# Kernel optimization log

Hardware: AMD Instinct MI355X
Metric: run time of the kernel (lower is better)

The kernel has to match this reference:

```python
import jax, jax.numpy as jnp
import numpy as np

BATCH, T, N = 64, 512, 1024

def setup_inputs() -> dict:
    key = jax.random.key(0)
    k1, k2, k3 = jax.random.split(key, 3)
    input_sequence = jax.random.normal(k1, (BATCH, T, N), dtype=jnp.float32)
    W_self_lower = jax.random.normal(k2, (N, N), dtype=jnp.float32) * 0.1
    W_input = jax.random.normal(k3, (N, N), dtype=jnp.float32) * 0.1
    return {"input_sequence": input_sequence, "W_self_lower": W_self_lower, "W_input": W_input}

def reference(input_sequence, W_self_lower, W_input):
    # W_self symmetric: (W + W.T)/2; note W_self.T == W_self
    W_self = (W_self_lower + W_self_lower.T) * 0.5
    batch = input_sequence.shape[0]
    n = W_self.shape[0]
    # Precompute input projection for all timesteps: (B, T, N) @ (N, N)^T
    x_proj = jnp.einsum('btn,mn->btm', input_sequence, W_input)
    h0 = jnp.zeros((batch, n), dtype=input_sequence.dtype)

    def step(h, xp_t):
        h_new = jnp.tanh(h @ W_self.T + xp_t)
        return h_new, h_new

    # scan over time axis: move T to leading axis
    _, states = jax.lax.scan(step, h0, jnp.swapaxes(x_proj, 0, 1))
    return jnp.swapaxes(states, 0, 1)  # (B, T, N)
```

## Files before the change

kernel.cpp:

```cpp
#include <hip/hip_runtime.h>
#include <hip/hip_bf16.h>
#include <cstdint>
#include <cmath>

constexpr int BATCH = 64;
constexpr int T     = 512;
constexpr int N     = 1024;
constexpr int NWG   = 256;
constexpr int NG    = 32;
constexpr int GM    = 16;

typedef float f4 __attribute__((ext_vector_type(4)));
typedef short bs8 __attribute__((ext_vector_type(8)));

struct alignas(128) PadInt { int v; int pad[31]; };
__device__ PadInt g_cnt[NG];
__device__ PadInt g_flag[NG];

__device__ __forceinline__ f4 ld_sys_x4(const float* p) {
  f4 v;
  asm volatile("global_load_dwordx4 %0, %1, off sc0 sc1" : "=v"(v) : "v"(p));
  return v;
}
__device__ __forceinline__ int ld_sys_i32(const int* p) {
  int v;
  asm volatile("global_load_dword %0, %1, off sc0 sc1\n\ts_waitcnt vmcnt(0)"
               : "=v"(v) : "v"(p) : "memory");
  return v;
}
__device__ __forceinline__ void st_sys_f32(float* p, float v) {
  asm volatile("global_store_dword %0, %1, off sc0 sc1 nt" ::"v"(p), "v"(v)
               : "memory");
}
__device__ __forceinline__ void wait_vm0(void) {
  asm volatile("s_waitcnt vmcnt(0)" ::: "memory");
  __builtin_amdgcn_sched_barrier(0);
}

__device__ __forceinline__ void arrive_cnt(int g, int t) {
  int old = __hip_atomic_fetch_add(&g_cnt[g].v, 1, __ATOMIC_RELAXED,
                                   __HIP_MEMORY_SCOPE_AGENT);
  if (old == t * GM + (GM - 1))
    __hip_atomic_store(&g_flag[g].v, t + 1, __ATOMIC_RELAXED,
                       __HIP_MEMORY_SCOPE_AGENT);
}
__device__ __forceinline__ void pollf(int g, int e) {
  while (ld_sys_i32(&g_flag[g].v) < e) __builtin_amdgcn_s_sleep(1);
}

__device__ __forceinline__ unsigned short f2bf(float f) {
  unsigned u = __builtin_bit_cast(unsigned, f);
  u = u + 0x7FFFu + ((u >> 16) & 1u);
  return (unsigned short)(u >> 16);
}
__device__ __forceinline__ float bf2f(unsigned short b) {
  unsigned u = ((unsigned)b) << 16;
  return __builtin_bit_cast(float, u);
}
__device__ __forceinline__ bs8 mk8hi(const float* p) {
  bs8 r;
#pragma unroll
  for (int j = 0; j < 8; ++j) r[j] = (short)f2bf(p[j]);
  return r;
}
__device__ __forceinline__ void mk8hilo(const float* p, bs8& hi, bs8& lo) {
  f4 a = *reinterpret_cast<const f4*>(p);
  f4 b = *reinterpret_cast<const f4*>(p + 4);
  float v[8] = {a[0], a[1], a[2], a[3], b[0], b[1], b[2], b[3]};
#pragma unroll
  for (int j = 0; j < 8; ++j) {
    unsigned short h = f2bf(v[j]);
    hi[j] = (short)h;
    lo[j] = (short)f2bf(v[j] - bf2f(h));
  }
}

__global__ __launch_bounds__(256) void symm_k(const float* __restrict__ W,
                                              float* __restrict__ Ws) {
  if (blockIdx.x == 0 && blockIdx.y == 0 && threadIdx.x < NG) {
    __hip_atomic_store(&g_cnt[threadIdx.x].v, 0, __ATOMIC_RELAXED,
                       __HIP_MEMORY_SCOPE_AGENT);
    __hip_atomic_store(&g_flag[threadIdx.x].v, 0, __ATOMIC_RELAXED,
                       __HIP_MEMORY_SCOPE_AGENT);
  }
  int j = blockIdx.x * 16 + (threadIdx.x & 15);
  int i = blockIdx.y * 16 + (threadIdx.x >> 4);
  Ws[(size_t)i * N + j] = 0.5f * (W[(size_t)i * N + j] + W[(size_t)j * N + i]);
}

__global__ __launch_bounds__(256) void xproj_gemm(const float* __restrict__ A,
                                                  const float* __restrict__ B,
                                                  float* __restrict__ C,
                                                  int M) {
  constexpr int BM = 128, BN = 128, BK = 16;
  __shared__ float As[BK][BM + 4];
  __shared__ float Bs[BK][BN + 4];

  const int tid = threadIdx.x;
  const int lin = blockIdx.x + gridDim.x * blockIdx.y;
  const int sw  = ((lin & 7) << 8) + (lin >> 3);
  const int bm  = sw >> 3;
  const int bn  = sw & 7;
  const int tx = tid & 15, ty = tid >> 4;
  const int K = N;

  float acc[8][8];
#pragma unroll
  for (int i = 0; i < 8; ++i)
#pragma unroll
    for (int j = 0; j < 8; ++j) acc[i][j] = 0.f;

  for (int kt = 0; kt < K; kt += BK) {
#pragma unroll
    for (int s = 0; s < 2; ++s) {
      int f = tid + s * 256;
      int row = f >> 2, kq = f & 3;
      float4 a = *reinterpret_cast<const float4*>(
          &A[(size_t)(bm * BM + row) * K + kt + kq * 4]);
      As[kq * 4 + 0][row] = a.x;
      As[kq * 4 + 1][row] = a.y;
      As[kq * 4 + 2][row] = a.z;
      As[kq * 4 + 3][row] = a.w;
      float4 b = *reinterpret_cast<const float4*>(
          &B[(size_t)(bn * BN + row) * K + kt + kq * 4]);
      Bs[kq * 4 + 0][row] = b.x;
      Bs[kq * 4 + 1][row] = b.y;
      Bs[kq * 4 + 2][row] = b.z;
      Bs[kq * 4 + 3][row] = b.w;
    }
    __syncthreads();

#pragma unroll
    for (int k = 0; k < BK; ++k) {
      float a[8], b[8];
      *reinterpret_cast<float4*>(&a[0]) =
          *reinterpret_cast<const float4*>(&As[k][ty * 8]);
      *reinterpret_cast<float4*>(&a[4]) =
          *reinterpret_cast<const float4*>(&As[k][ty * 8 + 4]);
      *reinterpret_cast<float4*>(&b[0]) =
          *reinterpret_cast<const float4*>(&Bs[k][tx * 8]);
      *reinterpret_cast<float4*>(&b[4]) =
          *reinterpret_cast<const float4*>(&Bs[k][tx * 8 + 4]);
#pragma unroll
      for (int i = 0; i < 8; ++i)
#pragma unroll
        for (int j = 0; j < 8; ++j) acc[i][j] = fmaf(a[i], b[j], acc[i][j]);
    }
    __syncthreads();
  }

#pragma unroll
  for (int i = 0; i < 8; ++i) {
    size_t row = (size_t)bm * BM + ty * 8 + i;
#pragma unroll
    for (int j = 0; j < 8; j += 4) {
      *reinterpret_cast<float4*>(&C[row * N + bn * BN + tx * 8 + j]) =
          *reinterpret_cast<const float4*>(&acc[i][j]);
    }
  }
}

__global__ __launch_bounds__(640, 1) void rnn_persist(
    float* __restrict__ out, const float* __restrict__ Ws) {
  const int tid = threadIdx.x;
  const int wg  = blockIdx.x;
  const int p   = wg & 15;
  const int cg  = wg >> 4;
  const int m0  = cg * 64;
  const int gA  = 2 * p, gB = 2 * p + 1;
  const int b0A = gA * 2, b0B = gB * 2;
  const size_t TN = (size_t)T * N;

  __shared__ __align__(16) short wloL[64][1032];
  __shared__ __align__(16) float hA[2][1028];
  __shared__ __align__(16) float hB[2][1028];
  __shared__ float xplA[128], xplB[128];
  __shared__ float redA[8 * 128], redB[8 * 128];
  __shared__ int lflags[64];

  if (tid == 0) {
    lflags[0] = -1; lflags[16] = -1;
    lflags[8] = 0;  lflags[24] = 0;
    lflags[32] = 0; lflags[48] = 0;
  }

  const int l = tid & 63;
  const int v = tid >> 6;

  for (int e = tid; e < 64 * 1024; e += 640) {
    int row = e >> 10, k = e & 1023;
    float x = Ws[(size_t)(m0 + row) * N + k];
    unsigned short hi = f2bf(x);
    wloL[row][k] = (short)f2bf(x - bf2f(hi));
  }
  bs8 whi[4][4];
  if (v < 8) {
#pragma unroll
    for (int mt = 0; mt < 4; ++mt)
#pragma unroll
      for (int kt = 0; kt < 4; ++kt)
        whi[mt][kt] = mk8hi(
            &Ws[(size_t)(m0 + 16 * mt + (l & 15)) * N + 128 * v + 32 * kt +
                8 * (l >> 4)]);
  }
  __syncthreads();

  if (v < 8) {
    const int n = l & 15;
    const int koff = 128 * v + 8 * (l >> 4);

    auto do_chain = [&](float (*hX)[1028], float* xplX, float* redX,
                        int rdyIdx, int wsIdx, int ackIdx, int b0, int t) {
      while (*(volatile int*)&lflags[rdyIdx] < t) __builtin_amdgcn_s_sleep(1);
      __builtin_amdgcn_fence(__ATOMIC_ACQUIRE, "workgroup");
      if (t > 0) {
        const float* hrow_ = &hX[n & 1][0];
        f4 acc0 = {0.f, 0.f, 0.f, 0.f}, acc1 = {0.f, 0.f, 0.f, 0.f};
        f4 acc2 = {0.f, 0.f, 0.f, 0.f}, acc3 = {0.f, 0.f, 0.f, 0.f};
#pragma unroll
        for (int kt = 0; kt < 4; ++kt) {
          bs8 bhi, blo;
          mk8hilo(hrow_ + koff + 32 * kt, bhi, blo);
          bs8 wl0 = *reinterpret_cast<const bs8*>(&wloL[n][koff + 32 * kt]);
          bs8 wl1 = *reinterpret_cast<const bs8*>(&wloL[16 + n][koff + 32 * kt]);
          bs8 wl2 = *reinterpret_cast<const bs8*>(&wloL[32 + n][koff + 32 * kt]);
          bs8 wl3 = *reinterpret_cast<const bs8*>(&wloL[48 + n][koff + 32 * kt]);
          acc0 = __builtin_amdgcn_mfma_f32_16x16x32_bf16(whi[0][kt], bhi, acc0, 0, 0, 0);
          acc0 = __builtin_amdgcn_mfma_f32_16x16x32_bf16(whi[0][kt], blo, acc0, 0, 0, 0);
          acc0 = __builtin_amdgcn_mfma_f32_16x16x32_bf16(wl0, bhi, acc0, 0, 0, 0);
          acc0 = __builtin_amdgcn_mfma_f32_16x16x32_bf16(wl0, blo, acc0, 0, 0, 0);
          acc1 = __builtin_amdgcn_mfma_f32_16x16x32_bf16(whi[1][kt], bhi, acc1, 0, 0, 0);
          acc1 = __builtin_amdgcn_mfma_f32_16x16x32_bf16(whi[1][kt], blo, acc1, 0, 0, 0);
          acc1 = __builtin_amdgcn_mfma_f32_16x16x32_bf16(wl1, bhi, acc1, 0, 0, 0);
          acc1 = __builtin_amdgcn_mfma_f32_16x16x32_bf16(wl1, blo, acc1, 0, 0, 0);
          acc2 = __builtin_amdgcn_mfma_f32_16x16x32_bf16(whi[2][kt], bhi, acc2, 0, 0, 0);
          acc2 = __builtin_amdgcn_mfma_f32_16x16x32_bf16(whi[2][kt], blo, acc2, 0, 0, 0);
          acc2 = __builtin_amdgcn_mfma_f32_16x16x32_bf16(wl2, bhi, acc2, 0, 0, 0);
          acc2 = __builtin_amdgcn_mfma_f32_16x16x32_bf16(wl2, blo, acc2, 0, 0, 0);
          acc3 = __builtin_amdgcn_mfma_f32_16x16x32_bf16(whi[3][kt], bhi, acc3, 0, 0, 0);
          acc3 = __builtin_amdgcn_mfma_f32_16x16x32_bf16(whi[3][kt], blo, acc3, 0, 0, 0);
          acc3 = __builtin_amdgcn_mfma_f32_16x16x32_bf16(wl3, bhi, acc3, 0, 0, 0);
          acc3 = __builtin_amdgcn_mfma_f32_16x16x32_bf16(wl3, blo, acc3, 0, 0, 0);
        }
        if (n < 2) {
          const int rb = 4 * (l >> 4);
#pragma unroll
          for (int r = 0; r < 4; ++r) {
            redX[v * 128 + (0  + rb + r) * 2 + n] = acc0[r];
            redX[v * 128 + (16 + rb + r) * 2 + n] = acc1[r];
            redX[v * 128 + (32 + rb + r) * 2 + n] = acc2[r];
            redX[v * 128 + (48 + rb + r) * 2 + n] = acc3[r];
          }
        }
      }
      __builtin_amdgcn_fence(__ATOMIC_RELEASE, "workgroup");
      if (l == 0) atomicAdd(&lflags[wsIdx], 1);
      if (v == 0) {
        while (*(volatile int*)&lflags[wsIdx] < 8 * (t + 1))
          __builtin_amdgcn_s_sleep(1);
        __builtin_amdgcn_fence(__ATOMIC_ACQUIRE, "workgroup");
        float pre0 = 0.f, pre1 = 0.f;
        if (t > 0) {
#pragma unroll
          for (int w = 0; w < 8; ++w) {
            pre0 += redX[w * 128 + l * 2 + 0];
            pre1 += redX[w * 128 + l * 2 + 1];
          }
        }
        float h0 = tanhf(pre0 + xplX[l]);
        float h1 = tanhf(pre1 + xplX[64 + l]);
        st_sys_f32(out + (size_t)(b0 + 0) * TN + (size_t)t * N + m0 + l, h0);
        st_sys_f32(out + (size_t)(b0 + 1) * TN + (size_t)t * N + m0 + l, h1);
        wait_vm0();
        if (l == 0) atomicAdd(&lflags[ackIdx], 1);
      }
    };

    for (int t = 0; t < T; ++t) {
      do_chain(hA, xplA, redA, 0, 8, 32, b0A, t);
      do_chain(hB, xplB, redB, 16, 24, 48, b0B, t);
    }
  } else {
    const bool isB = (v == 9);
    const int lane = l;
    const int g    = isB ? gB : gA;
    const int b0   = isB ? b0B : b0A;
    float (*hb)[1028] = isB ? hB : hA;
    float* xpl = isB ? xplB : xplA;
    volatile int* ready = isB ? (volatile int*)&lflags[16]
                              : (volatile int*)&lflags[0];
    volatile int* cnt = isB ? (volatile int*)&lflags[48]
                            : (volatile int*)&lflags[32];

    const int r = lane >> 5;
    const int c = lane & 31;
    const float* hrow = out + (size_t)(b0 + r) * TN;
    const int xr = lane >> 4, xc = (lane & 15) * 4;
    const float* xsrc = out + (size_t)(b0 + xr) * TN + m0 + xc;

    f4 xnext;
    {
      f4 xv;
      if (lane < 32) xv = ld_sys_x4(xsrc);
      wait_vm0();
      if (lane < 32) *reinterpret_cast<f4*>(&xpl[xr * 64 + xc]) = xv;
      __builtin_amdgcn_fence(__ATOMIC_RELEASE, "workgroup");
      if (lane == 0) *ready = 0;
      if (lane < 32) xnext = ld_sys_x4(xsrc + (size_t)N);
    }

    for (int t = 1; t < T; ++t) {
      if (lane == 0) {
        while (*cnt < t) __builtin_amdgcn_s_sleep(1);
        arrive_cnt(g, t - 1);
        pollf(g, t);
      }
      const float* hs = hrow + (size_t)(t - 1) * N;
      f4 tmp[8];
#pragma unroll
      for (int q = 0; q < 8; ++q) tmp[q] = ld_sys_x4(hs + 4 * (c + 32 * q));
      wait_vm0();
#pragma unroll
      for (int q = 0; q < 8; ++q)
        *reinterpret_cast<f4*>(&hb[r][4 * (c + 32 * q)]) = tmp[q];
      if (lane < 32) *reinterpret_cast<f4*>(&xpl[xr * 64 + xc]) = xnext;
      __builtin_amdgcn_fence(__ATOMIC_RELEASE, "workgroup");
      if (lane == 0) *ready = t;
      if (t + 1 < T && lane < 32)
        xnext = ld_sys_x4(xsrc + (size_t)(t + 1) * N);
    }
  }
}

extern "C" void kernel_launch(void* const* d_in, const int* in_sizes, int n_in,
                              void* d_out, int out_size, void* d_ws,
                              size_t ws_size, hipStream_t stream) {
  const float* in_seq  = (const float*)d_in[0];
  const float* W_lower = (const float*)d_in[1];
  const float* W_input = (const float*)d_in[2];
  float* out = (float*)d_out;
  float* Ws  = (float*)d_ws;

  symm_k<<<dim3(N / 16, N / 16), 256, 0, stream>>>(W_lower, Ws);
  xproj_gemm<<<dim3(N / 128, (BATCH * T) / 128), 256, 0, stream>>>(
      in_seq, W_input, out, BATCH * T);
  rnn_persist<<<NWG, 640, 0, stream>>>(out, Ws);
}
```

Before: 3.045 ms.

## Pre-split h into bf16 hi/lo in loader, drop lo*lo MFMA, fragment-order W lo

```diff
diff --git a/kernel.cpp b/kernel.cpp
--- a/kernel.cpp
+++ b/kernel.cpp
@@ -1,5 +1,4 @@
 #include <hip/hip_runtime.h>
-#include <hip/hip_bf16.h>
 #include <cstdint>
 #include <cmath>
 
@@ -11,6 +10,7 @@
 constexpr int GM    = 16;
 
 typedef float f4 __attribute__((ext_vector_type(4)));
+typedef short s4 __attribute__((ext_vector_type(4)));
 typedef short bs8 __attribute__((ext_vector_type(8)));
 
 struct alignas(128) PadInt { int v; int pad[31]; };
@@ -56,12 +56,6 @@
 __device__ __forceinline__ float bf2f(unsigned short b) {
   unsigned u = ((unsigned)b) << 16;
   return __builtin_bit_cast(float, u);
-}
-__device__ __forceinline__ bs8 mk8hi(const float* p) {
-  bs8 r;
-#pragma unroll
-  for (int j = 0; j < 8; ++j) r[j] = (short)f2bf(p[j]);
-  return r;
 }
 __device__ __forceinline__ void mk8hilo(const float* p, bs8& hi, bs8& lo) {
   f4 a = *reinterpret_cast<const f4*>(p);
@@ -171,9 +165,9 @@
   const int b0A = gA * 2, b0B = gB * 2;
   const size_t TN = (size_t)T * N;
 
-  __shared__ __align__(16) short wloL[64][1032];
-  __shared__ __align__(16) float hA[2][1028];
-  __shared__ __align__(16) float hB[2][1028];
+  __shared__ __align__(16) short wloF[65536];
+  __shared__ __align__(16) short hsA[4][1032];
+  __shared__ __align__(16) short hsB[4][1032];
   __shared__ float xplA[128], xplB[128];
   __shared__ float redA[8 * 128], redB[8 * 128];
   __shared__ int lflags[64];
@@ -186,64 +180,63 @@
 
   const int l = tid & 63;
   const int v = tid >> 6;
-
-  for (int e = tid; e < 64 * 1024; e += 640) {
-    int row = e >> 10, k = e & 1023;
-    float x = Ws[(size_t)(m0 + row) * N + k];
-    unsigned short hi = f2bf(x);
-    wloL[row][k] = (short)f2bf(x - bf2f(hi));
-  }
+  const int n = l & 15;
+  const int g = l >> 4;
+
   bs8 whi[4][4];
   if (v < 8) {
 #pragma unroll
     for (int mt = 0; mt < 4; ++mt)
 #pragma unroll
-      for (int kt = 0; kt < 4; ++kt)
-        whi[mt][kt] = mk8hi(
-            &Ws[(size_t)(m0 + 16 * mt + (l & 15)) * N + 128 * v + 32 * kt +
-                8 * (l >> 4)]);
+      for (int kt = 0; kt < 4; ++kt) {
+        bs8 hi, lo;
+        mk8hilo(&Ws[(size_t)(m0 + 16 * mt + n) * N + 128 * v + 32 * kt + 8 * g],
+                hi, lo);
+        whi[mt][kt] = hi;
+        *reinterpret_cast<bs8*>(
+            &wloF[((((v * 4 + mt) * 4 + kt) * 4 + g) * 16 + n) * 8]) = lo;
+      }
   }
   __syncthreads();
 
   if (v < 8) {
-    const int n = l & 15;
-    const int koff = 128 * v + 8 * (l >> 4);
-
-    auto do_chain = [&](float (*hX)[1028], float* xplX, float* redX,
+    const int koff = 128 * v + 8 * g;
+    const int hrow = n & 1;
+
+    auto do_chain = [&](short (*hsX)[1032], float* xplX, float* redX,
                         int rdyIdx, int wsIdx, int ackIdx, int b0, int t) {
       while (*(volatile int*)&lflags[rdyIdx] < t) __builtin_amdgcn_s_sleep(1);
       __builtin_amdgcn_fence(__ATOMIC_ACQUIRE, "workgroup");
       if (t > 0) {
-        const float* hrow_ = &hX[n & 1][0];
         f4 acc0 = {0.f, 0.f, 0.f, 0.f}, acc1 = {0.f, 0.f, 0.f, 0.f};
         f4 acc2 = {0.f, 0.f, 0.f, 0.f}, acc3 = {0.f, 0.f, 0.f, 0.f};
 #pragma unroll
         for (int kt = 0; kt < 4; ++kt) {
-          bs8 bhi, blo;
-          mk8hilo(hrow_ + koff + 32 * kt, bhi, blo);
-          bs8 wl0 = *reinterpret_cast<const bs8*>(&wloL[n][koff + 32 * kt]);
-          bs8 wl1 = *reinterpret_cast<const bs8*>(&wloL[16 + n][koff + 32 * kt]);
-          bs8 wl2 = *reinterpret_cast<const bs8*>(&wloL[32 + n][koff + 32 * kt]);
-          bs8 wl3 = *reinterpret_cast<const bs8*>(&wloL[48 + n][koff + 32 * kt]);
+          bs8 bhi = *reinterpret_cast<const bs8*>(&hsX[hrow][koff + 32 * kt]);
+          bs8 blo = *reinterpret_cast<const bs8*>(&hsX[2 + hrow][koff + 32 * kt]);
+          bs8 wl0 = *reinterpret_cast<const bs8*>(
+              &wloF[((((v * 4 + 0) * 4 + kt) * 4 + g) * 16 + n) * 8]);
+          bs8 wl1 = *reinterpret_cast<const bs8*>(
+              &wloF[((((v * 4 + 1) * 4 + kt) * 4 + g) * 16 + n) * 8]);
+          bs8 wl2 = *reinterpret_cast<const bs8*>(
+              &wloF[((((v * 4 + 2) * 4 + kt) * 4 + g) * 16 + n) * 8]);
+          bs8 wl3 = *reinterpret_cast<const bs8*>(
+              &wloF[((((v * 4 + 3) * 4 + kt) * 4 + g) * 16 + n) * 8]);
           acc0 = __builtin_amdgcn_mfma_f32_16x16x32_bf16(whi[0][kt], bhi, acc0, 0, 0, 0);
           acc0 = __builtin_amdgcn_mfma_f32_16x16x32_bf16(whi[0][kt], blo, acc0, 0, 0, 0);
           acc0 = __builtin_amdgcn_mfma_f32_16x16x32_bf16(wl0, bhi, acc0, 0, 0, 0);
-          acc0 = __builtin_amdgcn_mfma_f32_16x16x32_bf16(wl0, blo, acc0, 0, 0, 0);
           acc1 = __builtin_amdgcn_mfma_f32_16x16x32_bf16(whi[1][kt], bhi, acc1, 0, 0, 0);
           acc1 = __builtin_amdgcn_mfma_f32_16x16x32_bf16(whi[1][kt], blo, acc1, 0, 0, 0);
           acc1 = __builtin_amdgcn_mfma_f32_16x16x32_bf16(wl1, bhi, acc1, 0, 0, 0);
-          acc1 = __builtin_amdgcn_mfma_f32_16x16x32_bf16(wl1, blo, acc1, 0, 0, 0);
           acc2 = __builtin_amdgcn_mfma_f32_16x16x32_bf16(whi[2][kt], bhi, acc2, 0, 0, 0);
           acc2 = __builtin_amdgcn_mfma_f32_16x16x32_bf16(whi[2][kt], blo, acc2, 0, 0, 0);
           acc2 = __builtin_amdgcn_mfma_f32_16x16x32_bf16(wl2, bhi, acc2, 0, 0, 0);
-          acc2 = __builtin_amdgcn_mfma_f32_16x16x32_bf16(wl2, blo, acc2, 0, 0, 0);
           acc3 = __builtin_amdgcn_mfma_f32_16x16x32_bf16(whi[3][kt], bhi, acc3, 0, 0, 0);
           acc3 = __builtin_amdgcn_mfma_f32_16x16x32_bf16(whi[3][kt], blo, acc3, 0, 0, 0);
           acc3 = __builtin_amdgcn_mfma_f32_16x16x32_bf16(wl3, bhi, acc3, 0, 0, 0);
-          acc3 = __builtin_amdgcn_mfma_f32_16x16x32_bf16(wl3, blo, acc3, 0, 0, 0);
         }
         if (n < 2) {
-          const int rb = 4 * (l >> 4);
+          const int rb = 4 * g;
 #pragma unroll
           for (int r = 0; r < 4; ++r) {
             redX[v * 128 + (0  + rb + r) * 2 + n] = acc0[r];
@@ -277,15 +270,15 @@
     };
 
     for (int t = 0; t < T; ++t) {
-      do_chain(hA, xplA, redA, 0, 8, 32, b0A, t);
-      do_chain(hB, xplB, redB, 16, 24, 48, b0B, t);
+      do_chain(hsA, xplA, redA, 0, 8, 32, b0A, t);
+      do_chain(hsB, xplB, redB, 16, 24, 48, b0B, t);
     }
   } else {
     const bool isB = (v == 9);
     const int lane = l;
-    const int g    = isB ? gB : gA;
+    const int grp  = isB ? gB : gA;
     const int b0   = isB ? b0B : b0A;
-    float (*hb)[1028] = isB ? hB : hA;
+    short (*hsb)[1032] = isB ? hsB : hsA;
     float* xpl = isB ? xplB : xplA;
     volatile int* ready = isB ? (volatile int*)&lflags[16]
                               : (volatile int*)&lflags[0];
@@ -312,8 +305,8 @@
     for (int t = 1; t < T; ++t) {
       if (lane == 0) {
         while (*cnt < t) __builtin_amdgcn_s_sleep(1);
-        arrive_cnt(g, t - 1);
-        pollf(g, t);
+        arrive_cnt(grp, t - 1);
+        pollf(grp, t);
       }
       const float* hs = hrow + (size_t)(t - 1) * N;
       f4 tmp[8];
@@ -321,8 +314,18 @@
       for (int q = 0; q < 8; ++q) tmp[q] = ld_sys_x4(hs + 4 * (c + 32 * q));
       wait_vm0();
 #pragma unroll
-      for (int q = 0; q < 8; ++q)
-        *reinterpret_cast<f4*>(&hb[r][4 * (c + 32 * q)]) = tmp[q];
+      for (int q = 0; q < 8; ++q) {
+        s4 hi4, lo4;
+#pragma unroll
+        for (int j = 0; j < 4; ++j) {
+          float x = tmp[q][j];
+          unsigned short h = f2bf(x);
+          hi4[j] = (short)h;
+          lo4[j] = (short)f2bf(x - bf2f(h));
+        }
+        *reinterpret_cast<s4*>(&hsb[r][4 * (c + 32 * q)]) = hi4;
+        *reinterpret_cast<s4*>(&hsb[2 + r][4 * (c + 32 * q)]) = lo4;
+      }
       if (lane < 32) *reinterpret_cast<f4*>(&xpl[xr * 64 + xc]) = xnext;
       __builtin_amdgcn_fence(__ATOMIC_RELEASE, "workgroup");
       if (lane == 0) *ready = t;
```

Result: faster. 2.869 ms (-5.8%).
